# Kernel optimization log

Hardware: AMD Instinct MI355X
Metric: run time of the kernel (lower is better)

Reference implementation:

```python
import jax, jax.numpy as jnp
import numpy as np

B, C, H, W = 8, 96, 512, 96  # W == w_size (required by the view semantics)
EPS = 1e-5


def setup_inputs() -> dict:
    key = jax.random.key(0)
    ks = jax.random.split(key, 3)
    x = jax.random.normal(ks[0], (B, C, H, W), dtype=jnp.float32)
    bn_gamma = jnp.ones((C,), jnp.float32)
    bn_beta = jnp.zeros((C,), jnp.float32)
    bn_mean = jnp.zeros((C,), jnp.float32)   # BatchNorm running mean (eval mode)
    bn_var = jnp.ones((C,), jnp.float32)     # BatchNorm running var  (eval mode)
    qkv_w = jax.random.normal(ks[1], (3 * C, C), jnp.float32) * (1.0 / np.sqrt(C))
    qkv_b = jnp.zeros((3 * C,), jnp.float32)
    return {"x": x, "bn_gamma": bn_gamma, "bn_beta": bn_beta,
            "bn_mean": bn_mean, "bn_var": bn_var,
            "qkv_w": qkv_w, "qkv_b": qkv_b}


def reference(x, bn_gamma, bn_beta, bn_mean, bn_var, qkv_w, qkv_b):
    # BatchNorm2d (eval-mode affine normalize), fused scale/shift per channel
    inv = (bn_gamma / jnp.sqrt(bn_var + EPS))[:, None, None]
    xn = (x - bn_mean[:, None, None]) * inv + bn_beta[:, None, None]
    # 1x1 conv QKV projection: [b,c,h,w] -> [b,3c,h,w]
    qkv = jnp.einsum('bchw,oc->bohw', xn, qkv_w) + qkv_b[None, :, None, None]
    q, k, v = jnp.split(qkv, 3, axis=1)  # each [b,c,h,w]
    # per-row attention over the width axis (w == w_size)
    qp = jnp.transpose(q, (0, 2, 3, 1))  # [b,h,w,c]
    kp = jnp.transpose(k, (0, 2, 3, 1))  # [b,h,w,c]
    vp = jnp.transpose(v, (0, 2, 3, 1))  # [b,h,w,c]
    score = jnp.einsum('bhqc,bhkc->bhqk', qp, kp)  # [b,h,w,w]
    attn = jax.nn.softmax(score, axis=-1)
    xt = jnp.einsum('bhqk,bhkc->bhqc', attn, vp)   # [b,h,w,c]
    out = jnp.transpose(xt, (0, 3, 1, 2)) + x       # residual add, [b,c,h,w]
    return out
```

## Files before the change

kernel.cpp:

```cpp
#include <hip/hip_runtime.h>

#define C_ 96
#define H_ 512
#define W_ 96
#define HW_ 49152
#define CHW_ 4718592
#define PIT 104
#define REG 9984

typedef _Float16 f16x8 __attribute__((ext_vector_type(8)));
typedef _Float16 f16x4 __attribute__((ext_vector_type(4)));
typedef _Float16 f16x2 __attribute__((ext_vector_type(2)));
typedef float    f32x4 __attribute__((ext_vector_type(4)));
typedef int      i32x4 __attribute__((ext_vector_type(4)));

#define MFMA16 __builtin_amdgcn_mfma_f32_16x16x32_f16

#define BAR() do { __builtin_amdgcn_sched_barrier(0); \
                   asm volatile("s_waitcnt lgkmcnt(0)" ::: "memory"); \
                   __builtin_amdgcn_s_barrier(); \
                   __builtin_amdgcn_sched_barrier(0); } while (0)

__global__ void prep_kernel(const float* __restrict__ wq,
                            const float* __restrict__ gamma,
                            const float* __restrict__ beta,
                            const float* __restrict__ mean,
                            const float* __restrict__ var,
                            _Float16* __restrict__ whf,
                            float* __restrict__ inv,
                            float* __restrict__ shift)
{
    int i = blockIdx.x * 256 + threadIdx.x;
    if (i < 3 * C_ * C_) {
        int c = i % C_;
        float iv = gamma[c] * rsqrtf(var[c] + 1e-5f);
        whf[i] = (_Float16)(wq[i] * iv);
    }
    if (i < C_) {
        float iv = gamma[i] * rsqrtf(var[i] + 1e-5f);
        inv[i]   = iv;
        shift[i] = beta[i] - mean[i] * iv;
    }
}

__global__ void prep_bias(const float* __restrict__ wq,
                          const float* __restrict__ qkvb,
                          const float* __restrict__ shift,
                          float* __restrict__ bprime)
{
    const int o = (blockIdx.x * 256 + threadIdx.x) >> 6;
    const int l = threadIdx.x & 63;
    if (o >= 3 * C_) return;
    float p = wq[o * C_ + l] * shift[l];
    if (l < 32) p += wq[o * C_ + 64 + l] * shift[64 + l];
    #pragma unroll
    for (int d = 32; d >= 1; d >>= 1) p += __shfl_xor(p, d);
    if (l == 0) bprime[o] = p + qkvb[o];
}

__global__ void prep2_kernel(const float* __restrict__ wq,
                             const float* __restrict__ inv,
                             const float* __restrict__ bprime,
                             _Float16* __restrict__ atm,
                             float* __restrict__ g0)
{
    const int c = blockIdx.x;
    const int t = threadIdx.x;
    __shared__ float ldsk[C_];
    if (t < C_) ldsk[t] = wq[(C_ + t) * C_ + c];
    __syncthreads();
    const float ivc = inv[c];
    if (t < C_) {
        float acc = 0.f;
        #pragma unroll 8
        for (int o = 0; o < C_; ++o)
            acc += wq[o * C_ + t] * ldsk[o];
        atm[c * C_ + t] = (_Float16)(acc * ivc * inv[t]);
    }
    if (t >= 64) {
        const int l = t - 64;
        float p = bprime[l] * ldsk[l];
        if (l < 32) p += bprime[64 + l] * ldsk[64 + l];
        #pragma unroll
        for (int d = 32; d >= 1; d >>= 1) p += __shfl_xor(p, d);
        if (l == 0) g0[c] = p * ivc;
    }
}

__device__ __forceinline__ void xchg(const f32x4 v[6], float scale,
                                     int q4, int n16, f16x8 fr[3])
{
    int pq[6][2];
    #pragma unroll
    for (int nt = 0; nt < 6; ++nt) {
        #pragma unroll
        for (int jj = 0; jj < 2; ++jj) {
            f16x2 h;
            h[0] = (_Float16)(v[nt][2 * jj] * scale);
            h[1] = (_Float16)(v[nt][2 * jj + 1] * scale);
            pq[nt][jj] = __builtin_bit_cast(int, h);
        }
    }
    const int srcA = ((q4 & 1) << 5) | n16;
    const int srcB = srcA + 16;
    #pragma unroll
    for (int kk = 0; kk < 3; ++kk) {
        const int a0 = __shfl(pq[2 * kk][0], srcA), a1 = __shfl(pq[2 * kk][1], srcA);
        const int a2 = __shfl(pq[2 * kk][0], srcB), a3 = __shfl(pq[2 * kk][1], srcB);
        const int b0 = __shfl(pq[2 * kk + 1][0], srcA), b1 = __shfl(pq[2 * kk + 1][1], srcA);
        const int b2 = __shfl(pq[2 * kk + 1][0], srcB), b3 = __shfl(pq[2 * kk + 1][1], srcB);
        i32x4 u;
        u[0] = (q4 < 2) ? a0 : b0;
        u[1] = (q4 < 2) ? a1 : b1;
        u[2] = (q4 < 2) ? a2 : b2;
        u[3] = (q4 < 2) ? a3 : b3;
        fr[kk] = __builtin_bit_cast(f16x8, u);
    }
}

__global__ __launch_bounds__(384, 5) void attn_kernel(
    const float* __restrict__ x,
    const _Float16* __restrict__ whf,
    const _Float16* __restrict__ atm,
    const float* __restrict__ g0,
    const float* __restrict__ bprime,
    float* __restrict__ out)
{
    __shared__ __align__(16) _Float16 smem[2 * REG];
    _Float16* XN  = smem;
    _Float16* XNT = smem + REG;

    const int tid  = threadIdx.x;
    const int ws   = tid >> 6;
    const int lane = tid & 63;
    const int q4   = lane >> 4;
    const int n16  = lane & 15;
    const int w0   = 16 * ws + 4 * q4;
    const int qrow = 16 * ws + n16;

    const int bh = blockIdx.x;
    const size_t base = (size_t)(bh >> 9) * CHW_ + (size_t)(bh & 511) * W_;

    {
        f32x4 xr[6];
        #pragma unroll
        for (int t = 0; t < 6; ++t)
            xr[t] = *(const f32x4*)(x + base + (size_t)(16 * t + n16) * HW_ + w0);
        #pragma unroll
        for (int t = 0; t < 6; ++t) {
            const int c = 16 * t + n16;
            f16x4 pk;
            #pragma unroll
            for (int r = 0; r < 4; ++r) pk[r] = (_Float16)xr[t][r];
            *(f16x4*)(XNT + c * PIT + w0) = pk;
            #pragma unroll
            for (int r = 0; r < 4; ++r)
                XN[(w0 + r) * PIT + c] = (_Float16)xr[t][r];
        }
    }
    BAR();

    f32x4 gac[6];
    #pragma unroll
    for (int nt = 0; nt < 6; ++nt)
        gac[nt] = *(const f32x4*)(g0 + 16 * nt + 4 * q4);
    #pragma unroll
    for (int kk = 0; kk < 3; ++kk) {
        const f16x8 bfr = *(const f16x8*)(XN + qrow * PIT + 32 * kk + 8 * q4);
        #pragma unroll
        for (int nt = 0; nt < 6; ++nt) {
            const f16x8 afr = *(const f16x8*)(atm + (16 * nt + n16) * 96 + 32 * kk + 8 * q4);
            gac[nt] = MFMA16(afr, bfr, gac[nt], 0, 0, 0);
        }
    }
    f16x8 gf[3];
    xchg(gac, 1.0f, q4, n16, gf);

    f32x4 sacc[6];
    #pragma unroll
    for (int nt = 0; nt < 6; ++nt) sacc[nt] = f32x4{0.f, 0.f, 0.f, 0.f};
    #pragma unroll
    for (int kk = 0; kk < 3; ++kk) {
        #pragma unroll
        for (int nt = 0; nt < 6; ++nt) {
            const f16x8 afr = *(const f16x8*)(XN + (16 * nt + n16) * PIT + 32 * kk + 8 * q4);
            sacc[nt] = MFMA16(afr, gf[kk], sacc[nt], 0, 0, 0);
        }
    }

    float mr0 = sacc[0][0], mr1 = sacc[0][1], mr2 = sacc[0][2], mr3 = sacc[0][3];
    #pragma unroll
    for (int nt = 1; nt < 6; ++nt) {
        mr0 = fmaxf(mr0, sacc[nt][0]); mr1 = fmaxf(mr1, sacc[nt][1]);
        mr2 = fmaxf(mr2, sacc[nt][2]); mr3 = fmaxf(mr3, sacc[nt][3]);
    }
    float m = fmaxf(fmaxf(mr0, mr1), fmaxf(mr2, mr3));
    m = fmaxf(m, __shfl_xor(m, 16));
    m = fmaxf(m, __shfl_xor(m, 32));
    float sr0 = 0.f, sr1 = 0.f, sr2 = 0.f, sr3 = 0.f;
    #pragma unroll
    for (int nt = 0; nt < 6; ++nt) {
        sacc[nt][0] = __expf(sacc[nt][0] - m); sr0 += sacc[nt][0];
        sacc[nt][1] = __expf(sacc[nt][1] - m); sr1 += sacc[nt][1];
        sacc[nt][2] = __expf(sacc[nt][2] - m); sr2 += sacc[nt][2];
        sacc[nt][3] = __expf(sacc[nt][3] - m); sr3 += sacc[nt][3];
    }
    float s = (sr0 + sr1) + (sr2 + sr3);
    s += __shfl_xor(s, 16);
    s += __shfl_xor(s, 32);
    const float pinv = 1.0f / s;

    f16x8 pa[3];
    xchg(sacc, pinv, q4, n16, pa);

    f32x4 zac[6];
    #pragma unroll
    for (int nt = 0; nt < 6; ++nt) zac[nt] = f32x4{0.f, 0.f, 0.f, 0.f};
    #pragma unroll
    for (int kk = 0; kk < 3; ++kk) {
        #pragma unroll
        for (int nt = 0; nt < 6; ++nt) {
            const f16x8 afr = *(const f16x8*)(XNT + (16 * nt + n16) * PIT + 32 * kk + 8 * q4);
            zac[nt] = MFMA16(afr, pa[kk], zac[nt], 0, 0, 0);
        }
    }
    f16x8 zf[3];
    xchg(zac, 1.0f, q4, n16, zf);

    f32x4 oacc[6];
    #pragma unroll
    for (int ot = 0; ot < 6; ++ot)
        oacc[ot] = *(const f32x4*)(bprime + 192 + 16 * ot + 4 * q4);
    #pragma unroll
    for (int kk = 0; kk < 3; ++kk) {
        #pragma unroll
        for (int ot = 0; ot < 6; ++ot) {
            const f16x8 afr = *(const f16x8*)(whf + (192 + 16 * ot + n16) * 96 + 32 * kk + 8 * q4);
            oacc[ot] = MFMA16(afr, zf[kk], oacc[ot], 0, 0, 0);
        }
    }

    #pragma unroll
    for (int ot = 0; ot < 6; ++ot) {
        #pragma unroll
        for (int r = 0; r < 4; ++r) {
            const float xv = (float)XNT[(16 * ot + 4 * q4 + r) * PIT + qrow];
            out[base + (size_t)(16 * ot + 4 * q4 + r) * HW_ + qrow] =
                oacc[ot][r] + xv;
        }
    }
}

extern "C" void kernel_launch(void* const* d_in, const int* in_sizes, int n_in,
                              void* d_out, int out_size, void* d_ws, size_t ws_size,
                              hipStream_t stream)
{
    const float* x     = (const float*)d_in[0];
    const float* gamma = (const float*)d_in[1];
    const float* beta  = (const float*)d_in[2];
    const float* mean  = (const float*)d_in[3];
    const float* var   = (const float*)d_in[4];
    const float* qkvw  = (const float*)d_in[5];
    const float* qkvb  = (const float*)d_in[6];
    float* out = (float*)d_out;

    _Float16* whf    = (_Float16*)d_ws;
    float*    bprime = (float*)((char*)d_ws + 55296);
    _Float16* atm    = (_Float16*)((char*)d_ws + 56448);
    float*    g0v    = (float*)((char*)d_ws + 74880);
    float*    inv    = (float*)((char*)d_ws + 75264);
    float*    shf    = (float*)((char*)d_ws + 75648);

    prep_kernel<<<108, 256, 0, stream>>>(qkvw, gamma, beta, mean, var, whf, inv, shf);
    prep_bias <<<72, 256, 0, stream>>>(qkvw, qkvb, shf, bprime);
    prep2_kernel<<<96, 128, 0, stream>>>(qkvw, inv, bprime, atm, g0v);
    attn_kernel<<<4096, 384, 0, stream>>>(x, whf, atm, g0v, bprime, out);
}
```

Before: 325.2 us.

## Stage attention weights in LDS, merge prep kernels, add MFMA priority hints

The two weight matrices used in the attention kernel's first and last MFMA stages are now copied into shared memory once per block, instead of being read from global memory inside the MFMA loops. To pay for this, the block's LDS footprint roughly doubles and the launch-bounds occupancy hint drops from 5 to 3. MFMA sections are wrapped in s_setprio raises, and the residual read switches to a vectorized load from the row-major copy. The three prep kernels become two by merging the weight-scaling and bias kernels and recomputing the BatchNorm inverse inline, which removes one launch and the intermediate buffers.

Result: no change. 320.8 us (-1.4%).

```diff
diff --git a/kernel.cpp b/kernel.cpp
--- a/kernel.cpp
+++ b/kernel.cpp
@@ -21,45 +21,45 @@
                    __builtin_amdgcn_s_barrier(); \
                    __builtin_amdgcn_sched_barrier(0); } while (0)
 
-__global__ void prep_kernel(const float* __restrict__ wq,
-                            const float* __restrict__ gamma,
-                            const float* __restrict__ beta,
-                            const float* __restrict__ mean,
-                            const float* __restrict__ var,
-                            _Float16* __restrict__ whf,
-                            float* __restrict__ inv,
-                            float* __restrict__ shift)
-{
-    int i = blockIdx.x * 256 + threadIdx.x;
-    if (i < 3 * C_ * C_) {
-        int c = i % C_;
-        float iv = gamma[c] * rsqrtf(var[c] + 1e-5f);
-        whf[i] = (_Float16)(wq[i] * iv);
-    }
-    if (i < C_) {
-        float iv = gamma[i] * rsqrtf(var[i] + 1e-5f);
-        inv[i]   = iv;
-        shift[i] = beta[i] - mean[i] * iv;
-    }
-}
-
-__global__ void prep_bias(const float* __restrict__ wq,
-                          const float* __restrict__ qkvb,
-                          const float* __restrict__ shift,
-                          float* __restrict__ bprime)
-{
-    const int o = (blockIdx.x * 256 + threadIdx.x) >> 6;
-    const int l = threadIdx.x & 63;
-    if (o >= 3 * C_) return;
-    float p = wq[o * C_ + l] * shift[l];
-    if (l < 32) p += wq[o * C_ + 64 + l] * shift[64 + l];
-    #pragma unroll
-    for (int d = 32; d >= 1; d >>= 1) p += __shfl_xor(p, d);
-    if (l == 0) bprime[o] = p + qkvb[o];
+__device__ __forceinline__ float bn_inv(const float* g, const float* v, int c) {
+    return g[c] * rsqrtf(v[c] + 1e-5f);
+}
+
+__global__ void prepA_kernel(const float* __restrict__ wq,
+                             const float* __restrict__ gamma,
+                             const float* __restrict__ beta,
+                             const float* __restrict__ mean,
+                             const float* __restrict__ var,
+                             const float* __restrict__ qkvb,
+                             _Float16* __restrict__ whf,
+                             float* __restrict__ bprime)
+{
+    if (blockIdx.x < 108) {
+        int i = blockIdx.x * 256 + threadIdx.x;
+        if (i < 3 * C_ * C_) {
+            int c = i % C_;
+            whf[i] = (_Float16)(wq[i] * bn_inv(gamma, var, c));
+        }
+    } else {
+        const int j = (blockIdx.x - 108) * 256 + threadIdx.x;
+        const int o = j >> 6;
+        const int l = j & 63;
+        if (o >= 3 * C_) return;
+        const float sh0 = beta[l] - mean[l] * bn_inv(gamma, var, l);
+        float p = wq[o * C_ + l] * sh0;
+        if (l < 32) {
+            const float sh1 = beta[64 + l] - mean[64 + l] * bn_inv(gamma, var, 64 + l);
+            p += wq[o * C_ + 64 + l] * sh1;
+        }
+        #pragma unroll
+        for (int d = 32; d >= 1; d >>= 1) p += __shfl_xor(p, d);
+        if (l == 0) bprime[o] = p + qkvb[o];
+    }
 }
 
 __global__ void prep2_kernel(const float* __restrict__ wq,
-                             const float* __restrict__ inv,
+                             const float* __restrict__ gamma,
+                             const float* __restrict__ var,
                              const float* __restrict__ bprime,
                              _Float16* __restrict__ atm,
                              float* __restrict__ g0)
@@ -69,13 +69,13 @@
     __shared__ float ldsk[C_];
     if (t < C_) ldsk[t] = wq[(C_ + t) * C_ + c];
     __syncthreads();
-    const float ivc = inv[c];
+    const float ivc = bn_inv(gamma, var, c);
     if (t < C_) {
         float acc = 0.f;
         #pragma unroll 8
         for (int o = 0; o < C_; ++o)
             acc += wq[o * C_ + t] * ldsk[o];
-        atm[c * C_ + t] = (_Float16)(acc * ivc * inv[t]);
+        atm[c * C_ + t] = (_Float16)(acc * ivc * bn_inv(gamma, var, t));
     }
     if (t >= 64) {
         const int l = t - 64;
@@ -118,7 +118,7 @@
     }
 }
 
-__global__ __launch_bounds__(384, 5) void attn_kernel(
+__global__ __launch_bounds__(384, 3) void attn_kernel(
     const float* __restrict__ x,
     const _Float16* __restrict__ whf,
     const _Float16* __restrict__ atm,
@@ -126,9 +126,11 @@
     const float* __restrict__ bprime,
     float* __restrict__ out)
 {
-    __shared__ __align__(16) _Float16 smem[2 * REG];
+    __shared__ __align__(16) _Float16 smem[4 * REG];
     _Float16* XN  = smem;
     _Float16* XNT = smem + REG;
+    _Float16* WA  = smem + 2 * REG;
+    _Float16* WV  = smem + 3 * REG;
 
     const int tid  = threadIdx.x;
     const int ws   = tid >> 6;
@@ -140,6 +142,17 @@
 
     const int bh = blockIdx.x;
     const size_t base = (size_t)(bh >> 9) * CHW_ + (size_t)(bh & 511) * W_;
+
+    #pragma unroll
+    for (int i = 0; i < 6; ++i) {
+        const int idx = i * 384 + tid;
+        const int row = idx / 12, seg = idx % 12;
+        const f16x8 v = (row < 96)
+            ? *(const f16x8*)(atm + row * 96 + seg * 8)
+            : *(const f16x8*)(whf + (96 + row) * 96 + seg * 8);
+        _Float16* dst = (row < 96) ? (WA + row * PIT) : (WV + (row - 96) * PIT);
+        *(f16x8*)(dst + seg * 8) = v;
+    }
 
     {
         f32x4 xr[6];
@@ -164,21 +177,24 @@
     #pragma unroll
     for (int nt = 0; nt < 6; ++nt)
         gac[nt] = *(const f32x4*)(g0 + 16 * nt + 4 * q4);
+    __builtin_amdgcn_s_setprio(1);
     #pragma unroll
     for (int kk = 0; kk < 3; ++kk) {
         const f16x8 bfr = *(const f16x8*)(XN + qrow * PIT + 32 * kk + 8 * q4);
         #pragma unroll
         for (int nt = 0; nt < 6; ++nt) {
-            const f16x8 afr = *(const f16x8*)(atm + (16 * nt + n16) * 96 + 32 * kk + 8 * q4);
+            const f16x8 afr = *(const f16x8*)(WA + (16 * nt + n16) * PIT + 32 * kk + 8 * q4);
             gac[nt] = MFMA16(afr, bfr, gac[nt], 0, 0, 0);
         }
     }
+    __builtin_amdgcn_s_setprio(0);
     f16x8 gf[3];
     xchg(gac, 1.0f, q4, n16, gf);
 
     f32x4 sacc[6];
     #pragma unroll
     for (int nt = 0; nt < 6; ++nt) sacc[nt] = f32x4{0.f, 0.f, 0.f, 0.f};
+    __builtin_amdgcn_s_setprio(1);
     #pragma unroll
     for (int kk = 0; kk < 3; ++kk) {
         #pragma unroll
@@ -187,6 +203,7 @@
             sacc[nt] = MFMA16(afr, gf[kk], sacc[nt], 0, 0, 0);
         }
     }
+    __builtin_amdgcn_s_setprio(0);
 
     float mr0 = sacc[0][0], mr1 = sacc[0][1], mr2 = sacc[0][2], mr3 = sacc[0][3];
     #pragma unroll
@@ -216,6 +233,7 @@
     f32x4 zac[6];
     #pragma unroll
     for (int nt = 0; nt < 6; ++nt) zac[nt] = f32x4{0.f, 0.f, 0.f, 0.f};
+    __builtin_amdgcn_s_setprio(1);
     #pragma unroll
     for (int kk = 0; kk < 3; ++kk) {
         #pragma unroll
@@ -224,6 +242,7 @@
             zac[nt] = MFMA16(afr, pa[kk], zac[nt], 0, 0, 0);
         }
     }
+    __builtin_amdgcn_s_setprio(0);
     f16x8 zf[3];
     xchg(zac, 1.0f, q4, n16, zf);
 
@@ -231,23 +250,24 @@
     #pragma unroll
     for (int ot = 0; ot < 6; ++ot)
         oacc[ot] = *(const f32x4*)(bprime + 192 + 16 * ot + 4 * q4);
+    __builtin_amdgcn_s_setprio(1);
     #pragma unroll
     for (int kk = 0; kk < 3; ++kk) {
         #pragma unroll
         for (int ot = 0; ot < 6; ++ot) {
-            const f16x8 afr = *(const f16x8*)(whf + (192 + 16 * ot + n16) * 96 + 32 * kk + 8 * q4);
+            const f16x8 afr = *(const f16x8*)(WV + (16 * ot + n16) * PIT + 32 * kk + 8 * q4);
             oacc[ot] = MFMA16(afr, zf[kk], oacc[ot], 0, 0, 0);
         }
     }
+    __builtin_amdgcn_s_setprio(0);
 
     #pragma unroll
     for (int ot = 0; ot < 6; ++ot) {
-        #pragma unroll
-        for (int r = 0; r < 4; ++r) {
-            const float xv = (float)XNT[(16 * ot + 4 * q4 + r) * PIT + qrow];
+        const f16x4 xv4 = *(const f16x4*)(XN + qrow * PIT + 16 * ot + 4 * q4);
+        #pragma unroll
+        for (int r = 0; r < 4; ++r)
             out[base + (size_t)(16 * ot + 4 * q4 + r) * HW_ + qrow] =
-                oacc[ot][r] + xv;
-        }
+                oacc[ot][r] + (float)xv4[r];
     }
 }
 
@@ -268,11 +288,8 @@
     float*    bprime = (float*)((char*)d_ws + 55296);
     _Float16* atm    = (_Float16*)((char*)d_ws + 56448);
     float*    g0v    = (float*)((char*)d_ws + 74880);
-    float*    inv    = (float*)((char*)d_ws + 75264);
-    float*    shf    = (float*)((char*)d_ws + 75648);
-
-    prep_kernel<<<108, 256, 0, stream>>>(qkvw, gamma, beta, mean, var, whf, inv, shf);
-    prep_bias <<<72, 256, 0, stream>>>(qkvw, qkvb, shf, bprime);
-    prep2_kernel<<<96, 128, 0, stream>>>(qkvw, inv, bprime, atm, g0v);
+
+    prepA_kernel<<<180, 256, 0, stream>>>(qkvw, gamma, beta, mean, var, qkvb, whf, bprime);
+    prep2_kernel<<<96, 128, 0, stream>>>(qkvw, gamma, var, bprime, atm, g0v);
     attn_kernel<<<4096, 384, 0, stream>>>(x, whf, atm, g0v, bprime, out);
 }
```
